# Kernel optimization log

Hardware: AMD Instinct MI355X
Metric: run time of the kernel (lower is better)

The kernel has to match this reference:

```python
import jax, jax.numpy as jnp
import numpy as np

# t2t / fold constants (FuseFormer defaults)
K = 7      # kernel size
S = 3      # stride
P = 3      # padding
H, W = 60, 108          # fold output_size
LH = (H + 2 * P - K) // S + 1   # 20
LW = (W + 2 * P - K) // S + 1   # 36
NVECS = LH * LW                 # 720


def _patch_indices():
    # row[k, i] = k + S*i : row coordinate in the padded image for kernel offset k, window i
    row = jnp.arange(K)[:, None] + S * jnp.arange(LH)[None, :]   # [K, LH]
    col = jnp.arange(K)[:, None] + S * jnp.arange(LW)[None, :]   # [K, LW]
    R = row[:, None, :, None]   # [K,1,LH,1]
    C = col[None, :, None, :]   # [1,K,1,LW] -> broadcast [K,K,LH,LW]
    return R, C


def setup_inputs() -> dict:
    key = jax.random.key(0)
    ks = jax.random.split(key, 5)
    b, n, d, hd = 2, 5760, 512, 1960
    return {
        "x": jax.random.normal(ks[0], (b, n, d), dtype=jnp.float32),
        "W1": jax.random.normal(ks[1], (d, hd), dtype=jnp.float32) * 0.02,
        "b1": jax.random.normal(ks[2], (hd,), dtype=jnp.float32) * 0.02,
        "W2": jax.random.normal(ks[3], (hd, d), dtype=jnp.float32) * 0.02,
        "b2": jax.random.normal(ks[4], (d,), dtype=jnp.float32) * 0.02,
    }


def reference(x, W1, b1, W2, b2):
    b, n, d = x.shape
    h = x @ W1 + b1                      # [b, n, 1960]
    c = h.shape[-1]
    Cch = c // (K * K)                   # 40 channels
    B2 = (b * n) // NVECS                # folded batch

    R, Cc = _patch_indices()

    # fold(x): [B2, C*K*K, L] scatter-add (col2im) into padded image
    hf = h.reshape(B2, NVECS, c).transpose(0, 2, 1)            # [B2, c, L]
    hf = hf.reshape(B2, Cch, K, K, LH, LW)
    padded = jnp.zeros((B2, Cch, H + 2 * P, W + 2 * P), h.dtype)
    padded = padded.at[:, :, R, Cc].add(hf)
    folded = padded[:, :, P:P + H, P:P + W]                    # [B2, C, H, W]

    # fold(ones): overlap-count normalizer (batch-independent, compute once)
    ones6 = jnp.ones((1, 1, K, K, LH, LW), h.dtype)
    npad = jnp.zeros((1, 1, H + 2 * P, W + 2 * P), h.dtype)
    norm = npad.at[:, :, R, Cc].add(ones6)[:, :, P:P + H, P:P + W]

    y = folded / norm                                          # broadcast over channels

    # unfold: im2col gather of 7x7 patches
    ypad = jnp.pad(y, ((0, 0), (0, 0), (P, P), (P, P)))
    patches = ypad[:, :, R, Cc]                                # [B2, C, K, K, LH, LW]
    uf = patches.reshape(B2, c, NVECS).transpose(0, 2, 1).reshape(b, n, c)

    # conv2: ReLU -> (dropout=identity at eval) -> Linear -> (dropout)
    out = jnp.maximum(uf, 0) @ W2 + b2                         # [b, n, d]
    return out
```

## Files before the change

### kernel.cpp

```cpp
#include <hip/hip_runtime.h>
#include <hip/hip_bf16.h>

#define M_ROWS   11520
#define D_IN     512
#define HD       1960
#define HDP      2048
#define CPAD     52
#define K2       2080
#define B2C      16
#define NVECS    720
#define LH       20
#define LW       36
#define HH       60
#define WW       108
#define CCH      40

using bf16x8 = __attribute__((ext_vector_type(8))) short;
using f32x4  = __attribute__((ext_vector_type(4))) float;
using f4     = __attribute__((ext_vector_type(4))) float;
using su4    = __attribute__((ext_vector_type(4))) unsigned short;

__device__ __forceinline__ float bf2f(unsigned short u) {
    unsigned int x = ((unsigned int)u) << 16;
    return __builtin_bit_cast(float, x);
}
__device__ __forceinline__ unsigned short f2bf(float f) {
    unsigned int x = __builtin_bit_cast(unsigned int, f);
    unsigned int r = (x + 0x7fffu + ((x >> 16) & 1u)) >> 16;
    return (unsigned short)r;
}

__device__ __forceinline__ void gl_lds16(const unsigned short* g, unsigned short* l) {
    __builtin_amdgcn_global_load_lds(
        (const __attribute__((address_space(1))) unsigned int*)g,
        (__attribute__((address_space(3))) unsigned int*)l, 16, 0, 0);
}

__global__ __launch_bounds__(256) void prep(
    const float* __restrict__ x, const float* __restrict__ W1, const float* __restrict__ W2,
    unsigned short* __restrict__ xb, unsigned short* __restrict__ w1t,
    unsigned short* __restrict__ w2t)
{
    __shared__ unsigned short tile[32][33];
    int b = blockIdx.x, t = threadIdx.x;
    if (b < 5760) {
        int i = b * 256 + t;
        f4 v = ((const f4*)x)[i];
        su4 o;
        o.x = f2bf(v.x); o.y = f2bf(v.y); o.z = f2bf(v.z); o.w = f2bf(v.w);
        ((su4*)xb)[i] = o;
        return;
    }
    int tx = t & 31, ty = t >> 5;
    if (b < 6784) {
        int blk = b - 5760;
        int kt = blk & 15, nt = blk >> 4;
        int k0 = kt * 32, n0 = nt * 32;
#pragma unroll
        for (int p = 0; p < 4; p++) {
            int k = k0 + ty + p * 8;
            int n = n0 + tx;
            tile[ty + p * 8][tx] = (n < HD) ? f2bf(W1[k * HD + n]) : (unsigned short)0;
        }
        __syncthreads();
#pragma unroll
        for (int p = 0; p < 4; p++) {
            int n = n0 + ty + p * 8;
            int k = k0 + tx;
            w1t[n * 512 + k] = tile[tx][ty + p * 8];
        }
    } else {
        int blk = b - 6784;
        int kt = blk % 62, nt = blk / 62;
        int k0 = kt * 32, n0 = nt * 32;
#pragma unroll
        for (int p = 0; p < 4; p++) {
            int k = k0 + ty + p * 8;
            int n = n0 + tx;
            tile[ty + p * 8][tx] = (k < HD) ? f2bf(W2[k * 512 + n]) : (unsigned short)0;
        }
        __syncthreads();
#pragma unroll
        for (int p = 0; p < 4; p++) {
            int n = n0 + ty + p * 8;
            int k = k0 + tx;
            if (k < HD) {
                int cch = k / 49, kk = k - cch * 49;
                w2t[n * K2 + cch * CPAD + kk] = tile[tx][ty + p * 8];
            }
        }
    }
}

__global__ __launch_bounds__(256) void gemm1_blk(
    const unsigned short* __restrict__ A,
    const unsigned short* __restrict__ Bt,
    const float* __restrict__ bias,
    unsigned short* __restrict__ h_blk)
{
    __shared__ unsigned short sA[128 * 32];
    __shared__ unsigned short sB[128 * 32];
    const int lda = D_IN, ldb = D_IN;

    int g = (blockIdx.x & 7) * 180 + (blockIdx.x >> 3);
    int bx = g & 15, by = g >> 4;
    int t    = threadIdx.x;
    int w    = t >> 6;
    int lane = t & 63;
    int quad = lane >> 4;
    int l16  = lane & 15;
    int row0 = by * 128, col0 = bx * 128;
    int wr = (w >> 1) * 64, wc = (w & 1) * 64;

    int srow = t >> 2;
    int qb = ((t & 3) - ((srow >> 1) & 3)) & 3;
    const unsigned short* Ag = A  + (size_t)(row0 + srow) * lda + qb * 8;
    const unsigned short* Bg = Bt + (size_t)(col0 + srow) * ldb + qb * 8;
    unsigned short* lA0 = sA + t * 8;
    unsigned short* lA1 = sA + 2048 + t * 8;
    unsigned short* lB0 = sB + t * 8;
    unsigned short* lB1 = sB + 2048 + t * 8;

    int xq = (quad + ((l16 >> 1) & 3)) & 3;

    f32x4 acc[4][4] = {};

    for (int k0 = 0; k0 < D_IN; k0 += 32) {
        gl_lds16(Ag + k0, lA0);
        gl_lds16(Ag + (size_t)64 * lda + k0, lA1);
        gl_lds16(Bg + k0, lB0);
        gl_lds16(Bg + (size_t)64 * ldb + k0, lB1);
        __syncthreads();

        bf16x8 a[4], bfr[4];
#pragma unroll
        for (int i = 0; i < 4; i++)
            a[i] = *(const bf16x8*)(sA + (wr + i * 16 + l16) * 32 + xq * 8);
#pragma unroll
        for (int j = 0; j < 4; j++)
            bfr[j] = *(const bf16x8*)(sB + (wc + j * 16 + l16) * 32 + xq * 8);
#pragma unroll
        for (int i = 0; i < 4; i++)
#pragma unroll
            for (int j = 0; j < 4; j++)
                acc[i][j] = __builtin_amdgcn_mfma_f32_16x16x32_bf16(a[i], bfr[j], acc[i][j], 0, 0, 0);
        __syncthreads();
    }

    int rowterm[16];
#pragma unroll
    for (int i = 0; i < 4; i++)
#pragma unroll
        for (int r = 0; r < 4; r++) {
            int row = row0 + wr + i * 16 + quad * 4 + r;
            int bb = row / NVECS;
            int sp = row - bb * NVECS;
            rowterm[i * 4 + r] = bb * (CCH * NVECS * CPAD) + sp * CPAD;
        }

#pragma unroll
    for (int j = 0; j < 4; j++) {
        int col = col0 + wc + j * 16 + l16;
        if (col < HD) {
            int cch = col / 49, kk = col - cch * 49;
            int colterm = cch * (NVECS * CPAD) + kk;
            float bv = bias[col];
#pragma unroll
            for (int i = 0; i < 4; i++)
#pragma unroll
                for (int r = 0; r < 4; r++)
                    h_blk[(size_t)rowterm[i * 4 + r] + colterm] = f2bf(acc[i][j][r] + bv);
        }
    }
}

__global__ __launch_bounds__(256) void fold_unfold(
    const unsigned short* __restrict__ h_blk,
    unsigned short* __restrict__ uf)
{
    __shared__ unsigned short h_lds[12 * 36 * CPAD];
    __shared__ unsigned short y_lds[33 * WW];
    int bid  = blockIdx.x;
    int half = bid & 1;
    int cch  = (bid >> 1) % CCH;
    int b2   = bid / (CCH * 2);
    int tid  = threadIdx.x;

    int lh_base = half ? 8 : 0;
    int y0 = half ? 27 : 0;
    int ny = half ? 33 : 31;

    const su4* hsrc = (const su4*)(h_blk +
        ((size_t)(b2 * CCH + cch) * NVECS + lh_base * 36) * CPAD);
    su4* hd = (su4*)h_lds;
    for (int i = tid; i < 12 * 36 * CPAD / 4; i += 256)
        hd[i] = hsrc[i];
    __syncthreads();

    for (int idx = tid; idx < ny * WW; idx += 256) {
        int rr = idx / WW, c = idx - rr * WW;
        int r  = y0 + rr;
        int rp = r + 3, cp = c + 3;
        int q1 = rp / 3, rem1 = rp - q1 * 3;
        int q2 = cp / 3, rem2 = cp - q2 * 3;
        bool rv0 = (q1 <= 19);
        bool rv2 = (rem1 == 0) & (q1 >= 2);
        int sl0 = q1 - lh_base, sl1 = sl0 - 1, sl2 = sl0 - 2;
        int rofs0 = rem1 * 7, rofs1 = rofs0 + 21, rofs2 = rofs0 + 42;
        bool cv0 = (q2 <= 35);
        bool cv2 = (rem2 == 0) & (q2 >= 2);
        int lw0 = q2, lw1 = q2 - 1, lw2 = q2 - 2;
        int n1 = 1 + (int)rv0 + (int)rv2;
        int n2 = 1 + (int)cv0 + (int)cv2;
        float s = 0.0f;
#define FTERM(vr, sl, rofs, vc, lw, cofs) {                                   \
        bool vv = (vr) & (vc);                                                \
        int ad = vv ? (((sl) * 36 + (lw)) * CPAD + (rofs) + (cofs)) : 0;      \
        float val = bf2f(h_lds[ad]);                                          \
        s += vv ? val : 0.0f; }
        FTERM(rv0,  sl0, rofs0, cv0,  lw0, rem2)
        FTERM(rv0,  sl0, rofs0, true, lw1, rem2 + 3)
        FTERM(rv0,  sl0, rofs0, cv2,  lw2, rem2 + 6)
        FTERM(true, sl1, rofs1, cv0,  lw0, rem2)
        FTERM(true, sl1, rofs1, true, lw1, rem2 + 3)
        FTERM(true, sl1, rofs1, cv2,  lw2, rem2 + 6)
        FTERM(rv2,  sl2, rofs2, cv0,  lw0, rem2)
        FTERM(rv2,  sl2, rofs2, true, lw1, rem2 + 3)
        FTERM(rv2,  sl2, rofs2, cv2,  lw2, rem2 + 6)
#undef FTERM
        y_lds[idx] = f2bf(fmaxf(s / (float)(n1 * n2), 0.0f));
    }
    __syncthreads();

    int lh0 = 10 * half;
    for (int i = tid; i < 360 * 13; i += 256) {
        int ri = i / 13, q = i - ri * 13;
        int lh = lh0 + ri / 36;
        int lw = ri % 36;
        int rb = 3 * lh - 3, cb = 3 * lw - 3;
        int j0 = q * 4;
        su4 o;
#pragma unroll
        for (int e = 0; e < 4; e++) {
            int j = j0 + e;
            unsigned short val = 0;
            if (j < 49) {
                int k1 = j / 7, k2 = j - k1 * 7;
                int r = rb + k1, cc = cb + k2;
                if ((unsigned)r < (unsigned)HH && (unsigned)cc < (unsigned)WW)
                    val = y_lds[(r - y0) * WW + cc];
            }
            ((unsigned short*)&o)[e] = val;
        }
        int row = b2 * NVECS + lh * 36 + lw;
        *(su4*)(uf + (size_t)row * K2 + cch * CPAD + j0) = o;
    }
}

__global__ __launch_bounds__(256) void gemm2(
    const unsigned short* __restrict__ A,
    const unsigned short* __restrict__ Bt,
    const float* __restrict__ bias,
    float* __restrict__ C)
{
    __shared__ unsigned short sA[128 * 32];
    __shared__ unsigned short sB[64 * 32];
    const int lda = K2, ldb = K2, ldc = D_IN;

    int g = (blockIdx.x & 7) * 90 + (blockIdx.x >> 3);
    int bx = g & 7, by = g >> 3;
    int t    = threadIdx.x;
    int w    = t >> 6;
    int lane = t & 63;
    int quad = lane >> 4;
    int l16  = lane & 15;
    int row0 = by * 128, col0 = bx * 64;
    int wr = (w >> 1) * 64, wc = (w & 1) * 32;

    int srow = t >> 2;
    int qb = ((t & 3) - ((srow >> 1) & 3)) & 3;
    const unsigned short* Ag = A  + (size_t)(row0 + srow) * lda + qb * 8;
    const unsigned short* Bg = Bt + (size_t)(col0 + srow) * ldb + qb * 8;
    unsigned short* lA0 = sA + t * 8;
    unsigned short* lA1 = sA + 2048 + t * 8;
    unsigned short* lB0 = sB + t * 8;

    int xq = (quad + ((l16 >> 1) & 3)) & 3;

    f32x4 acc[4][2] = {};

    for (int k0 = 0; k0 < K2; k0 += 32) {
        gl_lds16(Ag + k0, lA0);
        gl_lds16(Ag + (size_t)64 * lda + k0, lA1);
        gl_lds16(Bg + k0, lB0);
        __syncthreads();

        bf16x8 a[4], bfr[2];
#pragma unroll
        for (int i = 0; i < 4; i++)
            a[i] = *(const bf16x8*)(sA + (wr + i * 16 + l16) * 32 + xq * 8);
#pragma unroll
        for (int j = 0; j < 2; j++)
            bfr[j] = *(const bf16x8*)(sB + (wc + j * 16 + l16) * 32 + xq * 8);
#pragma unroll
        for (int i = 0; i < 4; i++)
#pragma unroll
            for (int j = 0; j < 2; j++)
                acc[i][j] = __builtin_amdgcn_mfma_f32_16x16x32_bf16(a[i], bfr[j], acc[i][j], 0, 0, 0);
        __syncthreads();
    }

#pragma unroll
    for (int j = 0; j < 2; j++) {
        int col = col0 + wc + j * 16 + l16;
        float bv = bias[col];
#pragma unroll
        for (int i = 0; i < 4; i++) {
            int rbase = row0 + wr + i * 16 + quad * 4;
#pragma unroll
            for (int r = 0; r < 4; r++)
                C[(size_t)(rbase + r) * ldc + col] = acc[i][j][r] + bv;
        }
    }
}

extern "C" void kernel_launch(void* const* d_in, const int* in_sizes, int n_in,
                              void* d_out, int out_size, void* d_ws, size_t ws_size,
                              hipStream_t stream) {
    const float* x   = (const float*)d_in[0];
    const float* W1  = (const float*)d_in[1];
    const float* b1  = (const float*)d_in[2];
    const float* W2  = (const float*)d_in[3];
    const float* b2f = (const float*)d_in[4];
    float* out = (float*)d_out;

    unsigned short* ws    = (unsigned short*)d_ws;
    unsigned short* xb    = ws;
    unsigned short* h_blk = xb + (size_t)M_ROWS * D_IN;
    unsigned short* uf    = h_blk + (size_t)M_ROWS * K2;
    unsigned short* w1t   = uf + (size_t)M_ROWS * K2;
    unsigned short* w2t   = w1t + (size_t)HDP * D_IN;

    hipLaunchKernelGGL(prep, dim3(7776), dim3(256), 0, stream, x, W1, W2, xb, w1t, w2t);

    hipLaunchKernelGGL(gemm1_blk, dim3((M_ROWS / 128) * (HDP / 128)), dim3(256), 0, stream,
                       xb, w1t, b1, h_blk);

    hipLaunchKernelGGL(fold_unfold, dim3(B2C * CCH * 2), dim3(256), 0, stream, h_blk, uf);

    hipLaunchKernelGGL(gemm2, dim3((M_ROWS / 128) * (D_IN / 64)), dim3(256), 0, stream,
                       uf, w2t, b2f, out);
}
```

Baseline: 222.6 us.

## Double-buffer LDS tiles in both GEMM kernels to overlap loads with MFMA

Both GEMM kernels now keep two LDS buffers per operand. Each iteration issues the global-to-LDS load for the next K tile before running the MFMAs on the current one, with the first tile loaded before the loop. This is meant to hide global load latency behind matrix math instead of stalling on a barrier before every tile. In exchange, shared memory per block doubles, which may lower occupancy, and the end-of-iteration barrier still waits on outstanding loads.

```diff
diff --git a/kernel.cpp b/kernel.cpp
--- a/kernel.cpp
+++ b/kernel.cpp
@@ -98,9 +98,10 @@
     const float* __restrict__ bias,
     unsigned short* __restrict__ h_blk)
 {
-    __shared__ unsigned short sA[128 * 32];
-    __shared__ unsigned short sB[128 * 32];
+    __shared__ unsigned short sA[2 * 128 * 32];
+    __shared__ unsigned short sB[2 * 128 * 32];
     const int lda = D_IN, ldb = D_IN;
+    const int NT = D_IN / 32;
 
     int g = (blockIdx.x & 7) * 180 + (blockIdx.x >> 3);
     int bx = g & 15, by = g >> 4;
@@ -116,29 +117,38 @@
     int qb = ((t & 3) - ((srow >> 1) & 3)) & 3;
     const unsigned short* Ag = A  + (size_t)(row0 + srow) * lda + qb * 8;
     const unsigned short* Bg = Bt + (size_t)(col0 + srow) * ldb + qb * 8;
-    unsigned short* lA0 = sA + t * 8;
-    unsigned short* lA1 = sA + 2048 + t * 8;
-    unsigned short* lB0 = sB + t * 8;
-    unsigned short* lB1 = sB + 2048 + t * 8;
+    unsigned short* lA = sA + t * 8;
+    unsigned short* lB = sB + t * 8;
 
     int xq = (quad + ((l16 >> 1) & 3)) & 3;
 
     f32x4 acc[4][4] = {};
 
-    for (int k0 = 0; k0 < D_IN; k0 += 32) {
-        gl_lds16(Ag + k0, lA0);
-        gl_lds16(Ag + (size_t)64 * lda + k0, lA1);
-        gl_lds16(Bg + k0, lB0);
-        gl_lds16(Bg + (size_t)64 * ldb + k0, lB1);
-        __syncthreads();
+    gl_lds16(Ag, lA);
+    gl_lds16(Ag + (size_t)64 * lda, lA + 2048);
+    gl_lds16(Bg, lB);
+    gl_lds16(Bg + (size_t)64 * ldb, lB + 2048);
+    __syncthreads();
+
+    for (int it = 0; it < NT; ++it) {
+        int cur = it & 1, nxt = cur ^ 1;
+        if (it + 1 < NT) {
+            int k0n = (it + 1) * 32;
+            gl_lds16(Ag + k0n, lA + nxt * 4096);
+            gl_lds16(Ag + (size_t)64 * lda + k0n, lA + nxt * 4096 + 2048);
+            gl_lds16(Bg + k0n, lB + nxt * 4096);
+            gl_lds16(Bg + (size_t)64 * ldb + k0n, lB + nxt * 4096 + 2048);
+        }
+        const unsigned short* bA = sA + cur * 4096;
+        const unsigned short* bB = sB + cur * 4096;
 
         bf16x8 a[4], bfr[4];
 #pragma unroll
         for (int i = 0; i < 4; i++)
-            a[i] = *(const bf16x8*)(sA + (wr + i * 16 + l16) * 32 + xq * 8);
+            a[i] = *(const bf16x8*)(bA + (wr + i * 16 + l16) * 32 + xq * 8);
 #pragma unroll
         for (int j = 0; j < 4; j++)
-            bfr[j] = *(const bf16x8*)(sB + (wc + j * 16 + l16) * 32 + xq * 8);
+            bfr[j] = *(const bf16x8*)(bB + (wc + j * 16 + l16) * 32 + xq * 8);
 #pragma unroll
         for (int i = 0; i < 4; i++)
 #pragma unroll
@@ -263,9 +273,10 @@
     const float* __restrict__ bias,
     float* __restrict__ C)
 {
-    __shared__ unsigned short sA[128 * 32];
-    __shared__ unsigned short sB[64 * 32];
+    __shared__ unsigned short sA[2 * 128 * 32];
+    __shared__ unsigned short sB[2 * 64 * 32];
     const int lda = K2, ldb = K2, ldc = D_IN;
+    const int NT = K2 / 32;
 
     int g = (blockIdx.x & 7) * 90 + (blockIdx.x >> 3);
     int bx = g & 7, by = g >> 3;
@@ -281,27 +292,36 @@
     int qb = ((t & 3) - ((srow >> 1) & 3)) & 3;
     const unsigned short* Ag = A  + (size_t)(row0 + srow) * lda + qb * 8;
     const unsigned short* Bg = Bt + (size_t)(col0 + srow) * ldb + qb * 8;
-    unsigned short* lA0 = sA + t * 8;
-    unsigned short* lA1 = sA + 2048 + t * 8;
-    unsigned short* lB0 = sB + t * 8;
+    unsigned short* lA = sA + t * 8;
+    unsigned short* lB = sB + t * 8;
 
     int xq = (quad + ((l16 >> 1) & 3)) & 3;
 
     f32x4 acc[4][2] = {};
 
-    for (int k0 = 0; k0 < K2; k0 += 32) {
-        gl_lds16(Ag + k0, lA0);
-        gl_lds16(Ag + (size_t)64 * lda + k0, lA1);
-        gl_lds16(Bg + k0, lB0);
-        __syncthreads();
+    gl_lds16(Ag, lA);
+    gl_lds16(Ag + (size_t)64 * lda, lA + 2048);
+    gl_lds16(Bg, lB);
+    __syncthreads();
+
+    for (int it = 0; it < NT; ++it) {
+        int cur = it & 1, nxt = cur ^ 1;
+        if (it + 1 < NT) {
+            int k0n = (it + 1) * 32;
+            gl_lds16(Ag + k0n, lA + nxt * 4096);
+            gl_lds16(Ag + (size_t)64 * lda + k0n, lA + nxt * 4096 + 2048);
+            gl_lds16(Bg + k0n, lB + nxt * 2048);
+        }
+        const unsigned short* bA = sA + cur * 4096;
+        const unsigned short* bB = sB + cur * 2048;
 
         bf16x8 a[4], bfr[2];
 #pragma unroll
         for (int i = 0; i < 4; i++)
-            a[i] = *(const bf16x8*)(sA + (wr + i * 16 + l16) * 32 + xq * 8);
+            a[i] = *(const bf16x8*)(bA + (wr + i * 16 + l16) * 32 + xq * 8);
 #pragma unroll
         for (int j = 0; j < 2; j++)
-            bfr[j] = *(const bf16x8*)(sB + (wc + j * 16 + l16) * 32 + xq * 8);
+            bfr[j] = *(const bf16x8*)(bB + (wc + j * 16 + l16) * 32 + xq * 8);
 #pragma unroll
         for (int i = 0; i < 4; i++)
 #pragma unroll
```

After: 220.5 us. About the same (-0.9%).
